# Optimization experiments

Hardware: AMD Instinct MI355X
Metric: run time of the kernel (lower is better)

## Reference

```python
import jax, jax.numpy as jnp
import numpy as np

VOCAB, EMSIZE, NBINS = 50000, 300, 5
B, Q, D, L = 32, 16, 10, 1000
EPS = 1e-8
# numpy.histogram edges from self.bins = [-1.0, -0.5, 0, 0.5, 1.0, 1.0]
BIN_LO = np.array([-1.0, -0.5, 0.0, 0.5, 1.0], np.float32)
BIN_HI = np.array([-0.5, 0.0, 0.5, 1.0, 1.0], np.float32)


def setup_inputs() -> dict:
    key = jax.random.key(0)
    ks = jax.random.split(key, 12)
    return {
        "batch_queries": jax.random.randint(ks[0], (B, Q), 0, VOCAB),
        "batch_docs": jax.random.randint(ks[1], (B, D, L), 0, VOCAB),
        "embedding": jax.random.normal(ks[2], (VOCAB, EMSIZE), jnp.float32) * 0.1,
        "gate_w": jax.random.normal(ks[3], (1, EMSIZE), jnp.float32) * 0.05,
        "gate_b": jnp.zeros((1,), jnp.float32),
        "w1": jax.random.normal(ks[4], (1, NBINS), jnp.float32) * 0.3,
        "b1": jnp.zeros((1,), jnp.float32),
        "w2": jax.random.normal(ks[5], (1, 1), jnp.float32),
        "b2": jnp.zeros((1,), jnp.float32),
        "out_w": jax.random.normal(ks[6], (1, 1), jnp.float32),
        "out_b": jnp.zeros((1,), jnp.float32),
    }


def _histogram(cos):  # cos: [B, D, Q, L] -> counts [B, D, Q, NBINS]
    lo = jnp.asarray(BIN_LO)
    hi = jnp.asarray(BIN_HI)
    c = cos[..., None]  # [B, D, Q, L, 1]
    # bins 0..3 half-open [lo, hi); last bin closed [1.0, 1.0]
    in_bin = (c >= lo) & (c < hi)
    last = (c[..., -1] >= lo[-1]) & (c[..., -1] <= hi[-1])
    in_bin = in_bin.at[..., -1].set(last)
    return in_bin.astype(jnp.float32).sum(axis=-2)


def reference(batch_queries, batch_docs, embedding, gate_w, gate_b,
              w1, b1, w2, b2, out_w, out_b):
    emb_q = embedding[batch_queries]            # [B, Q, E]
    emb_d = embedding[batch_docs]               # [B, D, L, E]

    # gating network: Linear(E,1) then softmax over query terms
    gate_logits = jnp.einsum('bqe,oe->bq', emb_q, gate_w) + gate_b[0]
    term_weights = jax.nn.softmax(gate_logits, axis=-1)  # [B, Q]

    # cosine similarity between every query term and doc term
    w12 = jnp.einsum('bqe,bdle->bdql', emb_q, emb_d)     # [B, D, Q, L]
    nq = jnp.linalg.norm(emb_q, axis=-1)                 # [B, Q]
    nd = jnp.linalg.norm(emb_d, axis=-1)                 # [B, D, L]
    denom = jnp.maximum(nq[:, None, :, None] * nd[:, :, None, :], EPS)
    cos = w12 / denom                                    # [B, D, Q, L]

    hist = _histogram(cos)                               # [B, D, Q, NBINS]

    # ffnn: Linear(NBINS,1) -> Linear(1,1)
    h = jnp.einsum('bdqn,on->bdq', hist, w1) + b1[0]
    ffnn_out = h * w2[0, 0] + b2[0]                      # [B, D, Q]

    weighted = ffnn_out * term_weights[:, None, :]       # [B, D, Q]
    pooled = weighted.sum(axis=-1)                       # [B, D]
    score = pooled * out_w[0, 0] + out_b[0]
    return score                                         # [B, D]
```

## Files before the change

### kernel.cpp

```cpp
#include <hip/hip_runtime.h>
#include <hip/hip_fp16.h>
#include <math.h>

#define VOCAB_ 50000
#define B_ 32
#define Q_ 16
#define D_ 10
#define L_ 1000
#define E_ 300

#define NS_  4
#define TPS_ 250
#define RP_  320
#define G8_  40
#define CVU_ (VOCAB_ * G8_)

typedef _Float16 half8 __attribute__((ext_vector_type(8)));
typedef _Float16 h2_t  __attribute__((ext_vector_type(2)));

#if __has_builtin(__builtin_amdgcn_fdot2)
#define DOT2(a, b, c) __builtin_amdgcn_fdot2((a), (b), (c), false)
#else
#define DOT2(a, b, c) fmaf((float)(a)[0], (float)(b)[0], \
                      fmaf((float)(a)[1], (float)(b)[1], (c)))
#endif
#define SV2(v, i) __builtin_shufflevector((v), (v), 2*(i), 2*(i)+1)

__global__ __launch_bounds__(256) void drmm_cvt(
    const float* __restrict__ emb, _Float16* __restrict__ emb16)
{
    const int u = blockIdx.x * 256 + threadIdx.x;
    if (u >= CVU_) return;
    const int row = u / G8_;
    const int g   = u - row * G8_;
    half8 o;
    if (g < 37) {
        const float* src = emb + (size_t)row * E_ + 8 * g;
        const float4 a = *(const float4*)src;
        const float4 c = *(const float4*)(src + 4);
        o[0] = (_Float16)a.x; o[1] = (_Float16)a.y;
        o[2] = (_Float16)a.z; o[3] = (_Float16)a.w;
        o[4] = (_Float16)c.x; o[5] = (_Float16)c.y;
        o[6] = (_Float16)c.z; o[7] = (_Float16)c.w;
    } else if (g == 37) {
        const float4 a = *(const float4*)(emb + (size_t)row * E_ + 296);
        o[0] = (_Float16)a.x; o[1] = (_Float16)a.y;
        o[2] = (_Float16)a.z; o[3] = (_Float16)a.w;
        o[4] = (_Float16)0.f; o[5] = (_Float16)0.f;
        o[6] = (_Float16)0.f; o[7] = (_Float16)0.f;
    } else {
#pragma unroll
        for (int i = 0; i < 8; ++i) o[i] = (_Float16)0.f;
    }
    *(half8*)(emb16 + (size_t)row * RP_ + 8 * g) = o;
}

__global__ __launch_bounds__(256) void drmm_prep(
    const int* __restrict__ bq, const float* __restrict__ emb,
    const float* __restrict__ gate_w, const float* __restrict__ gate_b,
    const float* __restrict__ b1, const float* __restrict__ w2,
    const float* __restrict__ b2, const float* __restrict__ out_w,
    const float* __restrict__ out_b,
    float* __restrict__ wqBuf, float* __restrict__ nqBuf,
    float* __restrict__ score)
{
    const int b = blockIdx.x;
    const int tid = threadIdx.x;
    const int w = tid >> 6, lane = tid & 63;
    __shared__ float logits[Q_];

#pragma unroll
    for (int i = 0; i < 4; ++i) {
        const int q = w * 4 + i;
        const int tok = bq[b * Q_ + q];
        const float* row = emb + (size_t)tok * E_;
        float4 dv = *(const float4*)(row + 4 * lane);
        float4 gv = *(const float4*)(gate_w + 4 * lane);
        float pd = dv.x * gv.x + dv.y * gv.y + dv.z * gv.z + dv.w * gv.w;
        float ps = dv.x * dv.x + dv.y * dv.y + dv.z * dv.z + dv.w * dv.w;
        if (lane < 11) {
            float4 dv2 = *(const float4*)(row + 256 + 4 * lane);
            float4 gv2 = *(const float4*)(gate_w + 256 + 4 * lane);
            pd += dv2.x * gv2.x + dv2.y * gv2.y + dv2.z * gv2.z + dv2.w * gv2.w;
            ps += dv2.x * dv2.x + dv2.y * dv2.y + dv2.z * dv2.z + dv2.w * dv2.w;
        }
#pragma unroll
        for (int off = 32; off > 0; off >>= 1) {
            pd += __shfl_xor(pd, off);
            ps += __shfl_xor(ps, off);
        }
        if (lane == 0) {
            logits[q] = pd + gate_b[0];
            nqBuf[b * Q_ + q] = sqrtf(ps);
        }
    }
    __syncthreads();

    if (tid == 0) {
        float m = -1e30f;
        for (int q = 0; q < Q_; ++q) m = fmaxf(m, logits[q]);
        float e[Q_];
        float s = 0.f;
        for (int q = 0; q < Q_; ++q) { e[q] = expf(logits[q] - m); s += e[q]; }
        const float sc = out_w[0] * w2[0] / s;
        for (int q = 0; q < Q_; ++q) wqBuf[b * Q_ + q] = e[q] * sc;
    }
    if (tid < D_)
        score[b * D_ + tid] = out_w[0] * (w2[0] * b1[0] + b2[0]) + out_b[0];
}

__global__ __launch_bounds__(256, 2) void drmm_main_f16(
    const int* __restrict__ bq, const int* __restrict__ bdocs,
    const _Float16* __restrict__ emb16, const float* __restrict__ w1,
    const float* __restrict__ wqBuf, const float* __restrict__ nqBuf,
    float* __restrict__ score)
{
    const int ls = blockIdx.x;
    const int d  = blockIdx.y;
    const int b  = blockIdx.z;
    const int tid  = threadIdx.x;
    const int lane = tid & 63;
    const int w    = tid >> 6;

    __shared__ half8 qt[Q_ * G8_];
    __shared__ float wsum[4];

    for (int u = tid; u < Q_ * G8_; u += 256) {
        const int q = u / G8_;
        const int g = u - q * G8_;
        qt[u] = *(const half8*)(emb16 + (size_t)bq[b * Q_ + q] * RP_ + 8 * g);
    }
    __syncthreads();

    const int tok = bdocs[(b * D_ + d) * L_ + ls * TPS_ + min(tid, TPS_ - 1)];
    const _Float16* drow = emb16 + (size_t)tok * RP_;

    float acc[Q_];
#pragma unroll
    for (int q = 0; q < Q_; ++q) acc[q] = 0.f;
    float sq = 0.f;

#pragma unroll 8
    for (int g = 0; g < G8_; ++g) {
        const half8 dv = *(const half8*)(drow + 8 * g);
        const h2_t d0 = SV2(dv, 0), d1 = SV2(dv, 1),
                   d2 = SV2(dv, 2), d3 = SV2(dv, 3);
        sq = DOT2(d0, d0, DOT2(d1, d1, DOT2(d2, d2, DOT2(d3, d3, sq))));
#pragma unroll
        for (int q = 0; q < Q_; ++q) {
            const half8 qv = qt[q * G8_ + g];
            float t = DOT2(SV2(qv, 0), d0, acc[q]);
            t       = DOT2(SV2(qv, 1), d1, t);
            t       = DOT2(SV2(qv, 2), d2, t);
            acc[q]  = DOT2(SV2(qv, 3), d3, t);
        }
    }

    float total = 0.f;
    if (tid < TPS_) {
        const float nd = sqrtf(sq);
        const float w10 = w1[0], w11 = w1[1], w12 = w1[2],
                    w13 = w1[3], w14 = w1[4];
#pragma unroll
        for (int q = 0; q < Q_; ++q) {
            const float nqv = nqBuf[b * Q_ + q];
            const float wqv = wqBuf[b * Q_ + q];
            const float denom = fmaxf(nqv * nd, 1e-8f);
            const float a = acc[q];
            const float wv = (a < -denom)        ? 0.f
                           : (a < -0.5f * denom) ? w10
                           : (a < 0.f)           ? w11
                           : (a < 0.5f * denom)  ? w12
                           : (a < denom)         ? w13
                           : (a <= denom)        ? w14
                                                 : 0.f;
            total = fmaf(wqv, wv, total);
        }
    }

#pragma unroll
    for (int off = 32; off > 0; off >>= 1) total += __shfl_xor(total, off);
    if (lane == 0) wsum[w] = total;
    __syncthreads();
    if (tid == 0)
        atomicAdd(&score[b * D_ + d], wsum[0] + wsum[1] + wsum[2] + wsum[3]);
}

__global__ __launch_bounds__(256, 4) void drmm_main_f32(
    const int* __restrict__ bq, const int* __restrict__ bdocs,
    const float* __restrict__ emb, const float* __restrict__ w1,
    const float* __restrict__ wqBuf, const float* __restrict__ nqBuf,
    float* __restrict__ score)
{
    const int ls = blockIdx.x;
    const int d  = blockIdx.y;
    const int b  = blockIdx.z;
    const int tid  = threadIdx.x;
    const int lane = tid & 63;
    const int w    = tid >> 6;

    __shared__ float4 qt[Q_ * 76];
    __shared__ float wsum[4];

    for (int u = tid; u < Q_ * 76; u += 256) {
        const int q = u / 76;
        const int c = u - q * 76;
        float4 v = make_float4(0.f, 0.f, 0.f, 0.f);
        if (c < 75)
            v = *(const float4*)(emb + (size_t)bq[b * Q_ + q] * E_ + 4 * c);
        qt[u] = v;
    }
    __syncthreads();

    const int tok = bdocs[(b * D_ + d) * L_ + ls * TPS_ + min(tid, TPS_ - 1)];
    const float* drow = emb + (size_t)tok * E_;

    float acc[Q_];
#pragma unroll
    for (int q = 0; q < Q_; ++q) acc[q] = 0.f;
    float sqA = 0.f, sqB = 0.f;

#pragma unroll 9
    for (int g = 0; g < 37; ++g) {
        const float4 a  = *(const float4*)(drow + 8 * g);
        const float4 c4 = *(const float4*)(drow + 8 * g + 4);
        sqA = fmaf(a.x, a.x, fmaf(a.z, a.z, fmaf(c4.x, c4.x, fmaf(c4.z, c4.z, sqA))));
        sqB = fmaf(a.y, a.y, fmaf(a.w, a.w, fmaf(c4.y, c4.y, fmaf(c4.w, c4.w, sqB))));
#pragma unroll
        for (int q = 0; q < Q_; ++q) {
            const float4 qa = qt[q * 76 + 2 * g];
            const float4 qb = qt[q * 76 + 2 * g + 1];
            float t0 = fmaf(a.x, qa.x, fmaf(a.y, qa.y,
                       fmaf(a.z, qa.z, fmaf(a.w, qa.w, acc[q]))));
            acc[q]   = fmaf(c4.x, qb.x, fmaf(c4.y, qb.y,
                       fmaf(c4.z, qb.z, fmaf(c4.w, qb.w, t0))));
        }
    }
    {
        const float4 a = *(const float4*)(drow + 296);
        sqA = fmaf(a.x, a.x, fmaf(a.z, a.z, sqA));
        sqB = fmaf(a.y, a.y, fmaf(a.w, a.w, sqB));
#pragma unroll
        for (int q = 0; q < Q_; ++q) {
            const float4 qa = qt[q * 76 + 74];
            acc[q] = fmaf(a.x, qa.x, fmaf(a.y, qa.y,
                     fmaf(a.z, qa.z, fmaf(a.w, qa.w, acc[q]))));
        }
    }

    float total = 0.f;
    if (tid < TPS_) {
        const float nd = sqrtf(sqA + sqB);
        const float w10 = w1[0], w11 = w1[1], w12 = w1[2],
                    w13 = w1[3], w14 = w1[4];
#pragma unroll
        for (int q = 0; q < Q_; ++q) {
            const float nqv = nqBuf[b * Q_ + q];
            const float wqv = wqBuf[b * Q_ + q];
            const float denom = fmaxf(nqv * nd, 1e-8f);
            const float a = acc[q];
            const float wv = (a < -denom)        ? 0.f
                           : (a < -0.5f * denom) ? w10
                           : (a < 0.f)           ? w11
                           : (a < 0.5f * denom)  ? w12
                           : (a < denom)         ? w13
                           : (a <= denom)        ? w14
                                                 : 0.f;
            total = fmaf(wqv, wv, total);
        }
    }

#pragma unroll
    for (int off = 32; off > 0; off >>= 1) total += __shfl_xor(total, off);
    if (lane == 0) wsum[w] = total;
    __syncthreads();
    if (tid == 0)
        atomicAdd(&score[b * D_ + d], wsum[0] + wsum[1] + wsum[2] + wsum[3]);
}

extern "C" void kernel_launch(void* const* d_in, const int* in_sizes, int n_in,
                              void* d_out, int out_size, void* d_ws, size_t ws_size,
                              hipStream_t stream)
{
    const int*   bq     = (const int*)d_in[0];
    const int*   bdocs  = (const int*)d_in[1];
    const float* emb    = (const float*)d_in[2];
    const float* gate_w = (const float*)d_in[3];
    const float* gate_b = (const float*)d_in[4];
    const float* w1     = (const float*)d_in[5];
    const float* b1     = (const float*)d_in[6];
    const float* w2     = (const float*)d_in[7];
    const float* b2     = (const float*)d_in[8];
    const float* out_w  = (const float*)d_in[9];
    const float* out_b  = (const float*)d_in[10];

    float* score = (float*)d_out;
    float* wqBuf = (float*)d_ws;
    float* nqBuf = wqBuf + B_ * Q_;

    const size_t e16_off   = 4096;
    const size_t e16_bytes = (size_t)VOCAB_ * RP_ * sizeof(_Float16);
    const bool useF16 = ws_size >= e16_off + e16_bytes;
    _Float16* emb16 = (_Float16*)((char*)d_ws + e16_off);

    if (useF16)
        drmm_cvt<<<dim3((CVU_ + 255) / 256), dim3(256), 0, stream>>>(emb, emb16);

    drmm_prep<<<dim3(B_), dim3(256), 0, stream>>>(
        bq, emb, gate_w, gate_b, b1, w2, b2, out_w, out_b, wqBuf, nqBuf, score);

    if (useF16)
        drmm_main_f16<<<dim3(NS_, D_, B_), dim3(256), 0, stream>>>(
            bq, bdocs, emb16, w1, wqBuf, nqBuf, score);
    else
        drmm_main_f32<<<dim3(NS_, D_, B_), dim3(256), 0, stream>>>(
            bq, bdocs, emb, w1, wqBuf, nqBuf, score);
}
```

Measured before the change: 177.8 us.

## Split f16 main kernel's embedding dimension across warp pairs to raise occupancy

The f16 main kernel now gives each block 128 doc tokens and splits the 40 half8 groups between two warps per token (24 and 16 groups). Partial dot products and squared norms from the second half go through shared memory and are combined before the histogram weighting. Grid slices double to 8 and launch bounds rise to 8 blocks per CU, aiming at more waves in flight to hide gather latency. In exchange it adds an LDS exchange, an extra barrier, an unbalanced 24/16 split and idle tail threads in the last slice.

```diff
diff --git a/kernel.cpp b/kernel.cpp
--- a/kernel.cpp
+++ b/kernel.cpp
@@ -9,10 +9,11 @@
 #define L_ 1000
 #define E_ 300
 
-#define NS_  4
-#define TPS_ 250
+#define NS_  8
+#define TPB_ 128
 #define RP_  320
 #define G8_  40
+#define GSPL_ 24
 #define CVU_ (VOCAB_ * G8_)
 
 typedef _Float16 half8 __attribute__((ext_vector_type(8)));
@@ -109,9 +110,116 @@
         score[b * D_ + tid] = out_w[0] * (w2[0] * b1[0] + b2[0]) + out_b[0];
 }
 
-__global__ __launch_bounds__(256, 2) void drmm_main_f16(
+__global__ __launch_bounds__(256, 8) void drmm_main_f16(
     const int* __restrict__ bq, const int* __restrict__ bdocs,
     const _Float16* __restrict__ emb16, const float* __restrict__ w1,
+    const float* __restrict__ wqBuf, const float* __restrict__ nqBuf,
+    float* __restrict__ score)
+{
+    const int ls = blockIdx.x;
+    const int d  = blockIdx.y;
+    const int b  = blockIdx.z;
+    const int tid  = threadIdx.x;
+    const int lane = tid & 63;
+    const int w = __builtin_amdgcn_readfirstlane(tid >> 6);
+    const int h = w & 1;
+    const int slot = (w >> 1) * 64 + lane;
+
+    __shared__ half8 qt[Q_ * G8_];
+    __shared__ float part[TPB_][17];
+    __shared__ float wsum[4];
+
+    for (int u = tid; u < Q_ * G8_; u += 256) {
+        const int q = u / G8_;
+        const int g = u - q * G8_;
+        qt[u] = *(const half8*)(emb16 + (size_t)bq[b * Q_ + q] * RP_ + 8 * g);
+    }
+    __syncthreads();
+
+    const int l = ls * TPB_ + slot;
+    const bool active = (l < L_);
+    const int tok = bdocs[(b * D_ + d) * L_ + min(l, L_ - 1)];
+    const _Float16* drow = emb16 + (size_t)tok * RP_;
+
+    float acc[Q_];
+#pragma unroll
+    for (int q = 0; q < Q_; ++q) acc[q] = 0.f;
+    float sq = 0.f;
+
+    if (h == 0) {
+#pragma unroll 8
+        for (int g = 0; g < GSPL_; ++g) {
+            const half8 dv = *(const half8*)(drow + 8 * g);
+            const h2_t d0 = SV2(dv, 0), d1 = SV2(dv, 1),
+                       d2 = SV2(dv, 2), d3 = SV2(dv, 3);
+            sq = DOT2(d0, d0, DOT2(d1, d1, DOT2(d2, d2, DOT2(d3, d3, sq))));
+#pragma unroll
+            for (int q = 0; q < Q_; ++q) {
+                const half8 qv = qt[q * G8_ + g];
+                float t = DOT2(SV2(qv, 0), d0, acc[q]);
+                t       = DOT2(SV2(qv, 1), d1, t);
+                t       = DOT2(SV2(qv, 2), d2, t);
+                acc[q]  = DOT2(SV2(qv, 3), d3, t);
+            }
+        }
+    } else {
+#pragma unroll 8
+        for (int g = GSPL_; g < G8_; ++g) {
+            const half8 dv = *(const half8*)(drow + 8 * g);
+            const h2_t d0 = SV2(dv, 0), d1 = SV2(dv, 1),
+                       d2 = SV2(dv, 2), d3 = SV2(dv, 3);
+            sq = DOT2(d0, d0, DOT2(d1, d1, DOT2(d2, d2, DOT2(d3, d3, sq))));
+#pragma unroll
+            for (int q = 0; q < Q_; ++q) {
+                const half8 qv = qt[q * G8_ + g];
+                float t = DOT2(SV2(qv, 0), d0, acc[q]);
+                t       = DOT2(SV2(qv, 1), d1, t);
+                t       = DOT2(SV2(qv, 2), d2, t);
+                acc[q]  = DOT2(SV2(qv, 3), d3, t);
+            }
+        }
+    }
+
+    if (h == 1) {
+#pragma unroll
+        for (int q = 0; q < Q_; ++q) part[slot][q] = acc[q];
+        part[slot][16] = sq;
+    }
+    __syncthreads();
+
+    float total = 0.f;
+    if (h == 0 && active) {
+        const float nd = sqrtf(sq + part[slot][16]);
+        const float w10 = w1[0], w11 = w1[1], w12 = w1[2],
+                    w13 = w1[3], w14 = w1[4];
+#pragma unroll
+        for (int q = 0; q < Q_; ++q) {
+            const float nqv = nqBuf[b * Q_ + q];
+            const float wqv = wqBuf[b * Q_ + q];
+            const float denom = fmaxf(nqv * nd, 1e-8f);
+            const float a = acc[q] + part[slot][q];
+            const float wv = (a < -denom)        ? 0.f
+                           : (a < -0.5f * denom) ? w10
+                           : (a < 0.f)           ? w11
+                           : (a < 0.5f * denom)  ? w12
+                           : (a < denom)         ? w13
+                           : (a <= denom)        ? w14
+                                                 : 0.f;
+            total = fmaf(wqv, wv, total);
+        }
+    }
+
+#pragma unroll
+    for (int off = 32; off > 0; off >>= 1) total += __shfl_xor(total, off);
+    if (lane == 0) wsum[w] = total;
+    __syncthreads();
+    if (tid == 0)
+        atomicAdd(&score[b * D_ + d], wsum[0] + wsum[1] + wsum[2] + wsum[3]);
+}
+
+__global__ __launch_bounds__(256, 4) void drmm_main_f32(
+    const int* __restrict__ bq, const int* __restrict__ bdocs,
+    const float* __restrict__ emb, const float* __restrict__ w1,
     const float* __restrict__ wqBuf, const float* __restrict__ nqBuf,
     float* __restrict__ score)
 {
@@ -122,43 +230,58 @@
     const int lane = tid & 63;
     const int w    = tid >> 6;
 
-    __shared__ half8 qt[Q_ * G8_];
+    __shared__ float4 qt[Q_ * 76];
     __shared__ float wsum[4];
 
-    for (int u = tid; u < Q_ * G8_; u += 256) {
-        const int q = u / G8_;
-        const int g = u - q * G8_;
-        qt[u] = *(const half8*)(emb16 + (size_t)bq[b * Q_ + q] * RP_ + 8 * g);
-    }
-    __syncthreads();
-
-    const int tok = bdocs[(b * D_ + d) * L_ + ls * TPS_ + min(tid, TPS_ - 1)];
-    const _Float16* drow = emb16 + (size_t)tok * RP_;
+    for (int u = tid; u < Q_ * 76; u += 256) {
+        const int q = u / 76;
+        const int c = u - q * 76;
+        float4 v = make_float4(0.f, 0.f, 0.f, 0.f);
+        if (c < 75)
+            v = *(const float4*)(emb + (size_t)bq[b * Q_ + q] * E_ + 4 * c);
+        qt[u] = v;
+    }
+    __syncthreads();
+
+    const int tok = bdocs[(b * D_ + d) * L_ + ls * 250 + min(tid, 249)];
+    const float* drow = emb + (size_t)tok * E_;
 
     float acc[Q_];
 #pragma unroll
     for (int q = 0; q < Q_; ++q) acc[q] = 0.f;
-    float sq = 0.f;
-
-#pragma unroll 8
-    for (int g = 0; g < G8_; ++g) {
-        const half8 dv = *(const half8*)(drow + 8 * g);
-        const h2_t d0 = SV2(dv, 0), d1 = SV2(dv, 1),
-                   d2 = SV2(dv, 2), d3 = SV2(dv, 3);
-        sq = DOT2(d0, d0, DOT2(d1, d1, DOT2(d2, d2, DOT2(d3, d3, sq))));
+    float sqA = 0.f, sqB = 0.f;
+
+#pragma unroll 9
+    for (int g = 0; g < 37; ++g) {
+        const float4 a  = *(const float4*)(drow + 8 * g);
+        const float4 c4 = *(const float4*)(drow + 8 * g + 4);
+        sqA = fmaf(a.x, a.x, fmaf(a.z, a.z, fmaf(c4.x, c4.x, fmaf(c4.z, c4.z, sqA))));
+        sqB = fmaf(a.y, a.y, fmaf(a.w, a.w, fmaf(c4.y, c4.y, fmaf(c4.w, c4.w, sqB))));
 #pragma unroll
         for (int q = 0; q < Q_; ++q) {
-            const half8 qv = qt[q * G8_ + g];
-            float t = DOT2(SV2(qv, 0), d0, acc[q]);
-            t       = DOT2(SV2(qv, 1), d1, t);
-            t       = DOT2(SV2(qv, 2), d2, t);
-            acc[q]  = DOT2(SV2(qv, 3), d3, t);
+            const float4 qa = qt[q * 76 + 2 * g];
+            const float4 qb = qt[q * 76 + 2 * g + 1];
+            float t0 = fmaf(a.x, qa.x, fmaf(a.y, qa.y,
+                       fmaf(a.z, qa.z, fmaf(a.w, qa.w, acc[q]))));
+            acc[q]   = fmaf(c4.x, qb.x, fmaf(c4.y, qb.y,
+                       fmaf(c4.z, qb.z, fmaf(c4.w, qb.w, t0))));
+        }
+    }
+    {
+        const float4 a = *(const float4*)(drow + 296);
+        sqA = fmaf(a.x, a.x, fmaf(a.z, a.z, sqA));
+        sqB = fmaf(a.y, a.y, fmaf(a.w, a.w, sqB));
+#pragma unroll
+        for (int q = 0; q < Q_; ++q) {
+            const float4 qa = qt[q * 76 + 74];
+            acc[q] = fmaf(a.x, qa.x, fmaf(a.y, qa.y,
+                     fmaf(a.z, qa.z, fmaf(a.w, qa.w, acc[q]))));
         }
     }
 
     float total = 0.f;
-    if (tid < TPS_) {
-        const float nd = sqrtf(sq);
+    if (tid < 250) {
+        const float nd = sqrtf(sqA + sqB);
         const float w10 = w1[0], w11 = w1[1], w12 = w1[2],
                     w13 = w1[3], w14 = w1[4];
 #pragma unroll
@@ -186,98 +309,6 @@
         atomicAdd(&score[b * D_ + d], wsum[0] + wsum[1] + wsum[2] + wsum[3]);
 }
 
-__global__ __launch_bounds__(256, 4) void drmm_main_f32(
-    const int* __restrict__ bq, const int* __restrict__ bdocs,
-    const float* __restrict__ emb, const float* __restrict__ w1,
-    const float* __restrict__ wqBuf, const float* __restrict__ nqBuf,
-    float* __restrict__ score)
-{
-    const int ls = blockIdx.x;
-    const int d  = blockIdx.y;
-    const int b  = blockIdx.z;
-    const int tid  = threadIdx.x;
-    const int lane = tid & 63;
-    const int w    = tid >> 6;
-
-    __shared__ float4 qt[Q_ * 76];
-    __shared__ float wsum[4];
-
-    for (int u = tid; u < Q_ * 76; u += 256) {
-        const int q = u / 76;
-        const int c = u - q * 76;
-        float4 v = make_float4(0.f, 0.f, 0.f, 0.f);
-        if (c < 75)
-            v = *(const float4*)(emb + (size_t)bq[b * Q_ + q] * E_ + 4 * c);
-        qt[u] = v;
-    }
-    __syncthreads();
-
-    const int tok = bdocs[(b * D_ + d) * L_ + ls * TPS_ + min(tid, TPS_ - 1)];
-    const float* drow = emb + (size_t)tok * E_;
-
-    float acc[Q_];
-#pragma unroll
-    for (int q = 0; q < Q_; ++q) acc[q] = 0.f;
-    float sqA = 0.f, sqB = 0.f;
-
-#pragma unroll 9
-    for (int g = 0; g < 37; ++g) {
-        const float4 a  = *(const float4*)(drow + 8 * g);
-        const float4 c4 = *(const float4*)(drow + 8 * g + 4);
-        sqA = fmaf(a.x, a.x, fmaf(a.z, a.z, fmaf(c4.x, c4.x, fmaf(c4.z, c4.z, sqA))));
-        sqB = fmaf(a.y, a.y, fmaf(a.w, a.w, fmaf(c4.y, c4.y, fmaf(c4.w, c4.w, sqB))));
-#pragma unroll
-        for (int q = 0; q < Q_; ++q) {
-            const float4 qa = qt[q * 76 + 2 * g];
-            const float4 qb = qt[q * 76 + 2 * g + 1];
-            float t0 = fmaf(a.x, qa.x, fmaf(a.y, qa.y,
-                       fmaf(a.z, qa.z, fmaf(a.w, qa.w, acc[q]))));
-            acc[q]   = fmaf(c4.x, qb.x, fmaf(c4.y, qb.y,
-                       fmaf(c4.z, qb.z, fmaf(c4.w, qb.w, t0))));
-        }
-    }
-    {
-        const float4 a = *(const float4*)(drow + 296);
-        sqA = fmaf(a.x, a.x, fmaf(a.z, a.z, sqA));
-        sqB = fmaf(a.y, a.y, fmaf(a.w, a.w, sqB));
-#pragma unroll
-        for (int q = 0; q < Q_; ++q) {
-            const float4 qa = qt[q * 76 + 74];
-            acc[q] = fmaf(a.x, qa.x, fmaf(a.y, qa.y,
-                     fmaf(a.z, qa.z, fmaf(a.w, qa.w, acc[q]))));
-        }
-    }
-
-    float total = 0.f;
-    if (tid < TPS_) {
-        const float nd = sqrtf(sqA + sqB);
-        const float w10 = w1[0], w11 = w1[1], w12 = w1[2],
-                    w13 = w1[3], w14 = w1[4];
-#pragma unroll
-        for (int q = 0; q < Q_; ++q) {
-            const float nqv = nqBuf[b * Q_ + q];
-            const float wqv = wqBuf[b * Q_ + q];
-            const float denom = fmaxf(nqv * nd, 1e-8f);
-            const float a = acc[q];
-            const float wv = (a < -denom)        ? 0.f
-                           : (a < -0.5f * denom) ? w10
-                           : (a < 0.f)           ? w11
-                           : (a < 0.5f * denom)  ? w12
-                           : (a < denom)         ? w13
-                           : (a <= denom)        ? w14
-                                                 : 0.f;
-            total = fmaf(wqv, wv, total);
-        }
-    }
-
-#pragma unroll
-    for (int off = 32; off > 0; off >>= 1) total += __shfl_xor(total, off);
-    if (lane == 0) wsum[w] = total;
-    __syncthreads();
-    if (tid == 0)
-        atomicAdd(&score[b * D_ + d], wsum[0] + wsum[1] + wsum[2] + wsum[3]);
-}
-
 extern "C" void kernel_launch(void* const* d_in, const int* in_sizes, int n_in,
                               void* d_out, int out_size, void* d_ws, size_t ws_size,
                               hipStream_t stream)
@@ -313,6 +344,6 @@
         drmm_main_f16<<<dim3(NS_, D_, B_), dim3(256), 0, stream>>>(
             bq, bdocs, emb16, w1, wqBuf, nqBuf, score);
     else
-        drmm_main_f32<<<dim3(NS_, D_, B_), dim3(256), 0, stream>>>(
+        drmm_main_f32<<<dim3(4, D_, B_), dim3(256), 0, stream>>>(
             bq, bdocs, emb, w1, wqBuf, nqBuf, score);
 }
```

Measured after the change: 251.6 us. +41.5%, slower.

## Partition doc tokens by vocabulary range per block to improve embedding cache locality

Applied to the files above, without the earlier changes.

The f16 main kernel now launches 8 blocks per (batch, doc), one per vocabulary range. Each block scans all 1000 tokens, keeps only those in its range in a shared-memory list, and computes cosine histograms for them. The aim is that blocks running together touch a narrower slice of the f16 embedding table, so gathered rows hit in L2/MALL more often. The cost is the scan of all tokens in every block, an LDS atomic compaction, a variable amount of work per block, and smaller 128-thread blocks.

```diff
diff --git a/kernel.cpp b/kernel.cpp
--- a/kernel.cpp
+++ b/kernel.cpp
@@ -9,8 +9,8 @@
 #define L_ 1000
 #define E_ 300
 
-#define NS_  4
-#define TPS_ 250
+#define NR_    8
+#define RANGE_ (VOCAB_ / NR_)
 #define RP_  320
 #define G8_  40
 #define CVU_ (VOCAB_ * G8_)
@@ -109,58 +109,72 @@
         score[b * D_ + tid] = out_w[0] * (w2[0] * b1[0] + b2[0]) + out_b[0];
 }
 
-__global__ __launch_bounds__(256, 2) void drmm_main_f16(
+__global__ __launch_bounds__(128, 4) void drmm_main_f16(
     const int* __restrict__ bq, const int* __restrict__ bdocs,
     const _Float16* __restrict__ emb16, const float* __restrict__ w1,
     const float* __restrict__ wqBuf, const float* __restrict__ nqBuf,
     float* __restrict__ score)
 {
-    const int ls = blockIdx.x;
-    const int d  = blockIdx.y;
-    const int b  = blockIdx.z;
+    const int r = blockIdx.x;
+    const int d = blockIdx.y;
+    const int b = blockIdx.z;
     const int tid  = threadIdx.x;
     const int lane = tid & 63;
     const int w    = tid >> 6;
 
     __shared__ half8 qt[Q_ * G8_];
-    __shared__ float wsum[4];
-
-    for (int u = tid; u < Q_ * G8_; u += 256) {
+    __shared__ unsigned int list[L_];
+    __shared__ int cnt;
+    __shared__ float wsum[2];
+
+    if (tid == 0) cnt = 0;
+    for (int u = tid; u < Q_ * G8_; u += 128) {
         const int q = u / G8_;
         const int g = u - q * G8_;
         qt[u] = *(const half8*)(emb16 + (size_t)bq[b * Q_ + q] * RP_ + 8 * g);
     }
     __syncthreads();
 
-    const int tok = bdocs[(b * D_ + d) * L_ + ls * TPS_ + min(tid, TPS_ - 1)];
-    const _Float16* drow = emb16 + (size_t)tok * RP_;
-
-    float acc[Q_];
-#pragma unroll
-    for (int q = 0; q < Q_; ++q) acc[q] = 0.f;
-    float sq = 0.f;
+    const int base = (b * D_ + d) * L_;
+    for (int l = tid; l < L_; l += 128) {
+        const int tok = bdocs[base + l];
+        if (tok / RANGE_ == r) {
+            const int pos = atomicAdd(&cnt, 1);
+            list[pos] = (unsigned)tok;
+        }
+    }
+    __syncthreads();
+    const int n = cnt;
+
+    const float w10 = w1[0], w11 = w1[1], w12 = w1[2],
+                w13 = w1[3], w14 = w1[4];
+
+    float total = 0.f;
+    for (int k = tid; k < n; k += 128) {
+        const _Float16* drow = emb16 + (size_t)list[k] * RP_;
+
+        float acc[Q_];
+#pragma unroll
+        for (int q = 0; q < Q_; ++q) acc[q] = 0.f;
+        float sq = 0.f;
 
 #pragma unroll 8
-    for (int g = 0; g < G8_; ++g) {
-        const half8 dv = *(const half8*)(drow + 8 * g);
-        const h2_t d0 = SV2(dv, 0), d1 = SV2(dv, 1),
-                   d2 = SV2(dv, 2), d3 = SV2(dv, 3);
-        sq = DOT2(d0, d0, DOT2(d1, d1, DOT2(d2, d2, DOT2(d3, d3, sq))));
-#pragma unroll
-        for (int q = 0; q < Q_; ++q) {
-            const half8 qv = qt[q * G8_ + g];
-            float t = DOT2(SV2(qv, 0), d0, acc[q]);
-            t       = DOT2(SV2(qv, 1), d1, t);
-            t       = DOT2(SV2(qv, 2), d2, t);
-            acc[q]  = DOT2(SV2(qv, 3), d3, t);
-        }
-    }
-
-    float total = 0.f;
-    if (tid < TPS_) {
+        for (int g = 0; g < G8_; ++g) {
+            const half8 dv = *(const half8*)(drow + 8 * g);
+            const h2_t d0 = SV2(dv, 0), d1 = SV2(dv, 1),
+                       d2 = SV2(dv, 2), d3 = SV2(dv, 3);
+            sq = DOT2(d0, d0, DOT2(d1, d1, DOT2(d2, d2, DOT2(d3, d3, sq))));
+#pragma unroll
+            for (int q = 0; q < Q_; ++q) {
+                const half8 qv = qt[q * G8_ + g];
+                float t = DOT2(SV2(qv, 0), d0, acc[q]);
+                t       = DOT2(SV2(qv, 1), d1, t);
+                t       = DOT2(SV2(qv, 2), d2, t);
+                acc[q]  = DOT2(SV2(qv, 3), d3, t);
+            }
+        }
+
         const float nd = sqrtf(sq);
-        const float w10 = w1[0], w11 = w1[1], w12 = w1[2],
-                    w13 = w1[3], w14 = w1[4];
 #pragma unroll
         for (int q = 0; q < Q_; ++q) {
             const float nqv = nqBuf[b * Q_ + q];
@@ -183,7 +197,7 @@
     if (lane == 0) wsum[w] = total;
     __syncthreads();
     if (tid == 0)
-        atomicAdd(&score[b * D_ + d], wsum[0] + wsum[1] + wsum[2] + wsum[3]);
+        atomicAdd(&score[b * D_ + d], wsum[0] + wsum[1]);
 }
 
 __global__ __launch_bounds__(256, 4) void drmm_main_f32(
@@ -212,7 +226,7 @@
     }
     __syncthreads();
 
-    const int tok = bdocs[(b * D_ + d) * L_ + ls * TPS_ + min(tid, TPS_ - 1)];
+    const int tok = bdocs[(b * D_ + d) * L_ + ls * 250 + min(tid, 249)];
     const float* drow = emb + (size_t)tok * E_;
 
     float acc[Q_];
@@ -249,7 +263,7 @@
     }
 
     float total = 0.f;
-    if (tid < TPS_) {
+    if (tid < 250) {
         const float nd = sqrtf(sqA + sqB);
         const float w10 = w1[0], w11 = w1[1], w12 = w1[2],
                     w13 = w1[3], w14 = w1[4];
@@ -310,9 +324,9 @@
         bq, emb, gate_w, gate_b, b1, w2, b2, out_w, out_b, wqBuf, nqBuf, score);
 
     if (useF16)
-        drmm_main_f16<<<dim3(NS_, D_, B_), dim3(256), 0, stream>>>(
+        drmm_main_f16<<<dim3(NR_, D_, B_), dim3(128), 0, stream>>>(
             bq, bdocs, emb16, w1, wqBuf, nqBuf, score);
     else
-        drmm_main_f32<<<dim3(NS_, D_, B_), dim3(256), 0, stream>>>(
+        drmm_main_f32<<<dim3(4, D_, B_), dim3(256), 0, stream>>>(
             bq, bdocs, emb, w1, wqBuf, nqBuf, score);
 }
```

After: 210.4 us. 18.3% more time.
